# Performance work log

Hardware: AMD Instinct MI355X
Metric: run time of the kernel (lower is better)

The kernel has to match this reference:

```python
import jax, jax.numpy as jnp
import numpy as np

HEADS = 16
DIM_HEAD = 64
WINDOW = 16
TOPK_RATIO = 0.1
SCALE = DIM_HEAD ** -0.5


def setup_inputs() -> dict:
    key = jax.random.key(0)
    k1, k2, k3 = jax.random.split(key, 3)
    b, n, d = 2, 2048, 1024
    inner = HEADS * DIM_HEAD
    x = jax.random.normal(k1, (b, n, d), dtype=jnp.float32)
    W_qkv = jax.random.normal(k2, (d, 3 * inner), dtype=jnp.float32) * (d ** -0.5)
    W_out = jax.random.normal(k3, (inner, d), dtype=jnp.float32) * (inner ** -0.5)
    b_out = jnp.zeros((d,), dtype=jnp.float32)
    mask = jnp.ones((b, n), dtype=bool)
    return {"x": x, "W_qkv": W_qkv, "W_out": W_out, "b_out": b_out, "mask": mask}


def reference(x, W_qkv, W_out, b_out, mask):
    b, n, d = x.shape
    h, dh = HEADS, DIM_HEAD
    qkv = x @ W_qkv  # [b, n, 3*h*dh]
    q, k, v = jnp.split(qkv, 3, axis=-1)
    # [b, n, h, dh] -> [b, h, n, dh]
    q = q.reshape(b, n, h, dh).transpose(0, 2, 1, 3)
    k = k.reshape(b, n, h, dh).transpose(0, 2, 1, 3)
    v = v.reshape(b, n, h, dh).transpose(0, 2, 1, 3)

    dots = jnp.einsum('bhid,bhjd->bhij', q, k) * SCALE  # [b, h, n, n]
    NEG = -jnp.finfo(dots.dtype).max

    # sliding window mask: |i - j| <= WINDOW
    idx = jnp.arange(n)
    win = jnp.abs(idx[:, None] - idx[None, :]) <= WINDOW  # [n, n]
    dots = jnp.where(win[None, None], dots, NEG)

    # key padding mask [b, 1, 1, n]
    dots = jnp.where(mask[:, None, None, :], dots, NEG)

    # top-k masking (threshold from kth largest masked score)
    k_value = max(1, int(n * TOPK_RATIO))
    thr = jax.lax.top_k(dots, k_value)[0][..., -1:]  # [b, h, n, 1]
    dots = jnp.where(dots >= thr, dots, NEG)

    attn = jax.nn.softmax(dots, axis=-1)
    out = jnp.einsum('bhij,bhjd->bhid', attn, v)  # [b, h, n, dh]
    out = out.transpose(0, 2, 1, 3).reshape(b, n, h * dh)
    return out @ W_out + b_out
```

## Files before the change

kernel.cpp:

```cpp
#include <hip/hip_runtime.h>
#include <hip/hip_bf16.h>
#include <cstdint>
#include <cstddef>


typedef __hip_bfloat16 bf16;
typedef __attribute__((ext_vector_type(8))) short bf16x8;
typedef __attribute__((ext_vector_type(4))) float f32x4;

#define MFMA16(a, b, c) __builtin_amdgcn_mfma_f32_16x16x32_bf16((a), (b), (c), 0, 0, 0)

__device__ __forceinline__ unsigned short f2bu(float f) {
  return __bfloat16_as_ushort(__float2bfloat16(f));
}

__device__ __forceinline__ void async16(const void* g, void* lds) {
  __builtin_amdgcn_global_load_lds(
      (const __attribute__((address_space(1))) void*)g,
      (__attribute__((address_space(3))) void*)lds, 16, 0, 0);
}

__global__ __launch_bounds__(256) void prep_fused(const float* __restrict__ x,
                                                  const float* __restrict__ Wqkv,
                                                  const float* __restrict__ Wout,
                                                  bf16* __restrict__ xb,
                                                  bf16* __restrict__ wqkvt,
                                                  bf16* __restrict__ woutt) {
  __shared__ bf16 t[32][33];
  int bx = blockIdx.x, tid = threadIdx.x;
  if (bx < 4096) {
    int idx = (bx * 256 + tid) * 4;
    float4 v = *(const float4*)(x + idx);
    union { bf16 h[4]; uint2 u; } pk;
    pk.h[0] = __float2bfloat16(v.x);
    pk.h[1] = __float2bfloat16(v.y);
    pk.h[2] = __float2bfloat16(v.z);
    pk.h[3] = __float2bfloat16(v.w);
    *(uint2*)(xb + idx) = pk.u;
    return;
  }
  const float* W;
  bf16* Wt;
  int N, n0, k0;
  if (bx < 7168) {
    int L = bx - 4096;
    W = Wqkv; Wt = wqkvt; N = 3072;
    n0 = (L % 96) * 32; k0 = (L / 96) * 32;
  } else {
    int L = bx - 7168;
    W = Wout; Wt = woutt; N = 1024;
    n0 = (L & 31) * 32; k0 = (L >> 5) * 32;
  }
  int tx = tid & 31, ty = tid >> 5;
#pragma unroll
  for (int i = 0; i < 32; i += 8)
    t[ty + i][tx] = __float2bfloat16(W[(size_t)(k0 + ty + i) * N + n0 + tx]);
  __syncthreads();
#pragma unroll
  for (int i = 0; i < 32; i += 8)
    Wt[(size_t)(n0 + ty + i) * 1024 + k0 + tx] = t[tx][ty + i];
}

__global__ __launch_bounds__(256, 3) void gemm1_qkv(const bf16* __restrict__ A,
                                                    const bf16* __restrict__ Bt,
                                                    bf16* __restrict__ qkv) {
  const int K = 1024;
  __shared__ __align__(16) bf16 sA[128 * 32];
  __shared__ __align__(16) bf16 sB[128 * 32];
  __shared__ __align__(16) unsigned short sE[4][64 * 68];
  int L = blockIdx.x, xcd = L & 7, s = L >> 3;
  int by = (xcd >> 1) * 8 + s / 12;
  int bx = (xcd & 1) * 12 + s % 12;
  int row0 = by * 128, col0 = bx * 128;
  int tid = threadIdx.x, wave = tid >> 6, lane = tid & 63;
  int wr = wave >> 1, wc = wave & 1;
  int q = lane >> 4, l16 = lane & 15;
  f32x4 acc[4][4] = {};
  for (int k0 = 0; k0 < K; k0 += 32) {
    __syncthreads();
#pragma unroll
    for (int p = 0; p < 2; ++p) {
      int off = (wave * 2 + p) * 1024 + lane * 16;
      int r = off >> 6, cb = off & 63;
      async16(A + (size_t)(row0 + r) * K + k0 + (cb >> 1), (char*)sA + (wave * 2 + p) * 1024);
      async16(Bt + (size_t)(col0 + r) * K + k0 + (cb >> 1), (char*)sB + (wave * 2 + p) * 1024);
    }
    __syncthreads();
    bf16x8 af[4], bfr[4];
#pragma unroll
    for (int mi = 0; mi < 4; ++mi)
      af[mi] = *(const bf16x8*)&sA[(wr * 64 + mi * 16 + l16) * 32 + q * 8];
#pragma unroll
    for (int ni = 0; ni < 4; ++ni)
      bfr[ni] = *(const bf16x8*)&sB[(wc * 64 + ni * 16 + l16) * 32 + q * 8];
#pragma unroll
    for (int mi = 0; mi < 4; ++mi)
#pragma unroll
      for (int ni = 0; ni < 4; ++ni)
        acc[mi][ni] = MFMA16(af[mi], bfr[ni], acc[mi][ni]);
  }
  unsigned short* ep = sE[wave];
#pragma unroll
  for (int mi = 0; mi < 4; ++mi)
#pragma unroll
    for (int ni = 0; ni < 4; ++ni)
#pragma unroll
      for (int t = 0; t < 4; ++t)
        ep[(mi * 16 + q * 4 + t) * 68 + ni * 16 + l16] = f2bu(acc[mi][ni][t]);
  __syncthreads();
  const size_t TS = (size_t)2 * 16 * 2048 * 64;
  int c_base = col0 + wc * 64;
  int which = c_base >> 10, rc = c_base & 1023, h = rc >> 6;
  int r_base = row0 + wr * 64;
  int b = r_base >> 11, i_base = r_base & 2047;
  bf16* dst = qkv + (size_t)which * TS + (((size_t)(b * 16 + h)) * 2048 + i_base) * 64;
  int lr = lane >> 3, lc = lane & 7;
#pragma unroll
  for (int pass = 0; pass < 8; ++pass) {
    int row = pass * 8 + lr;
    uint4 val = *(const uint4*)&ep[row * 68 + lc * 8];
    *(uint4*)(dst + (size_t)row * 64 + lc * 8) = val;
  }
}

__global__ __launch_bounds__(256) void gemm2_out(const bf16* __restrict__ A,
                                                 const bf16* __restrict__ Bt,
                                                 const float* __restrict__ bias,
                                                 float* __restrict__ out) {
  const int K = 1024, N = 1024;
  __shared__ __align__(16) bf16 sA[128 * 32];
  __shared__ __align__(16) bf16 sB[64 * 32];
  int L = blockIdx.x, xcd = L & 7, s = L >> 3;
  int by = (xcd >> 1) * 8 + (s >> 3);
  int bx = (xcd & 1) * 8 + (s & 7);
  int row0 = by * 128, col0 = bx * 64;
  int tid = threadIdx.x, wave = tid >> 6, lane = tid & 63;
  int wr = wave >> 1, wc = wave & 1;
  int q = lane >> 4, l16 = lane & 15;
  f32x4 acc[4][2] = {};
  for (int k0 = 0; k0 < K; k0 += 32) {
    __syncthreads();
#pragma unroll
    for (int p = 0; p < 2; ++p) {
      int off = (wave * 2 + p) * 1024 + lane * 16;
      int r = off >> 6, cb = off & 63;
      async16(A + (size_t)(row0 + r) * K + k0 + (cb >> 1), (char*)sA + (wave * 2 + p) * 1024);
    }
    {
      int off = wave * 1024 + lane * 16;
      int r = off >> 6, cb = off & 63;
      async16(Bt + (size_t)(col0 + r) * K + k0 + (cb >> 1), (char*)sB + wave * 1024);
    }
    __syncthreads();
    bf16x8 af[4], bfr[2];
#pragma unroll
    for (int mi = 0; mi < 4; ++mi)
      af[mi] = *(const bf16x8*)&sA[(wr * 64 + mi * 16 + l16) * 32 + q * 8];
#pragma unroll
    for (int ni = 0; ni < 2; ++ni)
      bfr[ni] = *(const bf16x8*)&sB[(wc * 32 + ni * 16 + l16) * 32 + q * 8];
#pragma unroll
    for (int mi = 0; mi < 4; ++mi)
#pragma unroll
      for (int ni = 0; ni < 2; ++ni)
        acc[mi][ni] = MFMA16(af[mi], bfr[ni], acc[mi][ni]);
  }
#pragma unroll
  for (int mi = 0; mi < 4; ++mi) {
#pragma unroll
    for (int ni = 0; ni < 2; ++ni) {
      int c = col0 + wc * 32 + ni * 16 + l16;
      float bv = bias[c];
#pragma unroll
      for (int t = 0; t < 4; ++t) {
        int r = row0 + wr * 64 + mi * 16 + q * 4 + t;
        out[(size_t)r * N + c] = acc[mi][ni][t] + bv;
      }
    }
  }
}

__global__ __launch_bounds__(256, 4) void attn_mfma(const bf16* __restrict__ qkv,
                                                    bf16* __restrict__ aout) {
  __shared__ __align__(16) unsigned short sQ[64 * 72];
  __shared__ __align__(16) unsigned short sK[96 * 72];
  __shared__ __align__(16) unsigned short sVt[64 * 120];

  int tid = threadIdx.x, wave = tid >> 6, lane = tid & 63;
  int quad = lane >> 4, l16 = lane & 15;
  int bh = blockIdx.x >> 5, qb = blockIdx.x & 31;
  int i0 = qb * 64, jbase = i0 - 16;
  const size_t TS = (size_t)32 * 2048 * 64;
  const bf16* qbase = qkv + (size_t)bh * 2048 * 64;
  const bf16* kbase = qbase + TS;
  const bf16* vbase = qbase + 2 * TS;

#pragma unroll
  for (int u = tid; u < 512; u += 256) {
    int row = u >> 3, cg = u & 7;
    uint4 val = *(const uint4*)(qbase + (size_t)(i0 + row) * 64 + cg * 8);
    *(uint4*)&sQ[row * 72 + cg * 8] = val;
  }
#pragma unroll
  for (int u = tid; u < 768; u += 256) {
    int slot = u >> 3, cg = u & 7;
    int j = jbase + slot;
    uint4 val = make_uint4(0, 0, 0, 0);
    if ((unsigned)j < 2048u) val = *(const uint4*)(kbase + (size_t)j * 64 + cg * 8);
    *(uint4*)&sK[slot * 72 + cg * 8] = val;
  }
#pragma unroll
  for (int u = tid; u < 768; u += 256) {
    int slot = u >> 3, cg = u & 7;
    int j = jbase + slot;
    union { uint4 v; unsigned short s[8]; } pk;
    pk.v = make_uint4(0, 0, 0, 0);
    if ((unsigned)j < 2048u) pk.v = *(const uint4*)(vbase + (size_t)j * 64 + cg * 8);
#pragma unroll
    for (int d = 0; d < 8; ++d) sVt[(cg * 8 + d) * 120 + slot] = pk.s[d];
  }
  {
    int d = tid >> 2, s0 = 96 + (tid & 3) * 4;
    *(uint2*)&sVt[d * 120 + s0] = make_uint2(0, 0);
  }
  __syncthreads();

  int m0 = wave * 16;
  bf16x8 aq[2];
#pragma unroll
  for (int ks = 0; ks < 2; ++ks)
    aq[ks] = *(const bf16x8*)&sQ[(m0 + l16) * 72 + ks * 32 + quad * 8];
  f32x4 s[3] = {};
#pragma unroll
  for (int nt = 0; nt < 3; ++nt)
#pragma unroll
    for (int ks = 0; ks < 2; ++ks) {
      bf16x8 bk = *(const bf16x8*)&sK[(m0 + nt * 16 + l16) * 72 + ks * 32 + quad * 8];
      s[nt] = MFMA16(aq[ks], bk, s[nt]);
    }

  float rinv[4];
#pragma unroll
  for (int t = 0; t < 4; ++t) {
    int r = quad * 4 + t;
    float mx = -INFINITY;
#pragma unroll
    for (int nt = 0; nt < 3; ++nt) {
      int cl = nt * 16 + l16;
      int j = jbase + m0 + cl;
      bool valid = ((unsigned)(cl - r) <= 32u) && ((unsigned)j < 2048u);
      float v = valid ? s[nt][t] * 0.125f : -INFINITY;
      s[nt][t] = v;
      mx = fmaxf(mx, v);
    }
#pragma unroll
    for (int msk = 8; msk; msk >>= 1) mx = fmaxf(mx, __shfl_xor(mx, msk));
    float sum = 0.f;
#pragma unroll
    for (int nt = 0; nt < 3; ++nt) {
      float ev = __expf(s[nt][t] - mx);
      s[nt][t] = ev;
      sum += ev;
    }
#pragma unroll
    for (int msk = 8; msk; msk >>= 1) sum += __shfl_xor(sum, msk);
    rinv[t] = 1.0f / sum;
  }

  unsigned short* sPw = &sQ[m0 * 72];
#pragma unroll
  for (int t = 0; t < 4; ++t) {
#pragma unroll
    for (int nt = 0; nt < 3; ++nt)
      sPw[(quad * 4 + t) * 72 + nt * 16 + l16] = f2bu(s[nt][t]);
    sPw[(quad * 4 + t) * 72 + 48 + l16] = 0;
  }

  bf16x8 ap[2];
#pragma unroll
  for (int ks = 0; ks < 2; ++ks)
    ap[ks] = *(const bf16x8*)&sPw[l16 * 72 + ks * 32 + quad * 8];
  f32x4 o[4] = {};
#pragma unroll
  for (int dt = 0; dt < 4; ++dt)
#pragma unroll
    for (int ks = 0; ks < 2; ++ks) {
      bf16x8 bv = *(const bf16x8*)&sVt[(dt * 16 + l16) * 120 + m0 + ks * 32 + quad * 8];
      o[dt] = MFMA16(ap[ks], bv, o[dt]);
    }

  int b = bh >> 4, h = bh & 15;
#pragma unroll
  for (int dt = 0; dt < 4; ++dt)
#pragma unroll
    for (int t = 0; t < 4; ++t) {
      int r = i0 + m0 + quad * 4 + t;
      aout[((size_t)(b * 2048 + r)) * 1024 + h * 64 + dt * 16 + l16] =
          __float2bfloat16(o[dt][t] * rinv[t]);
    }
}

extern "C" void kernel_launch(void* const* d_in, const int* in_sizes, int n_in,
                              void* d_out, int out_size, void* d_ws, size_t ws_size,
                              hipStream_t stream) {
  const float* x = (const float*)d_in[0];
  const float* Wqkv = (const float*)d_in[1];
  const float* Wout = (const float*)d_in[2];
  const float* bout = (const float*)d_in[3];

  char* ws = (char*)d_ws;
  bf16* xb = (bf16*)(ws);
  bf16* wqkvt = (bf16*)(ws + 8388608);
  bf16* woutt = (bf16*)(ws + 14680064);
  bf16* qkvb = (bf16*)(ws + 16777216);
  bf16* aout = xb;

  hipLaunchKernelGGL(prep_fused, dim3(8192), dim3(256), 0, stream, x, Wqkv, Wout, xb, wqkvt, woutt);
  hipLaunchKernelGGL(gemm1_qkv, dim3(768), dim3(256), 0, stream, xb, wqkvt, qkvb);
  hipLaunchKernelGGL(attn_mfma, dim3(1024), dim3(256), 0, stream, qkvb, aout);
  hipLaunchKernelGGL(gemm2_out, dim3(512), dim3(256), 0, stream, aout, woutt, bout,
                     (float*)d_out);
}
```

Baseline: 149.5 us.

## Double K-step to 64 with XOR-swizzled LDS tiles in both GEMMs

Both GEMM kernels now load a 64-wide K slice per iteration into 128-byte rows whose 16-byte chunks are XOR-swizzled by row. This halves the barrier count per K and avoids LDS bank conflicts on the fragment reads. The per-lane global source pointers are precomputed once, and the QKV epilogue staging buffer is halved by writing in two phases so the larger tiles still fit at 3 blocks/CU. gemm2 also gains a launch-bounds occupancy hint. The cost is more LDS per block, which could limit occupancy.

```diff
diff --git a/kernel.cpp b/kernel.cpp
--- a/kernel.cpp
+++ b/kernel.cpp
@@ -65,9 +65,9 @@
                                                     const bf16* __restrict__ Bt,
                                                     bf16* __restrict__ qkv) {
   const int K = 1024;
-  __shared__ __align__(16) bf16 sA[128 * 32];
-  __shared__ __align__(16) bf16 sB[128 * 32];
-  __shared__ __align__(16) unsigned short sE[4][64 * 68];
+  __shared__ __align__(16) char sA[128 * 128];
+  __shared__ __align__(16) char sB[128 * 128];
+  __shared__ __align__(16) unsigned short sE[4][32 * 68];
   int L = blockIdx.x, xcd = L & 7, s = L >> 3;
   int by = (xcd >> 1) * 8 + s / 12;
   int bx = (xcd & 1) * 12 + s % 12;
@@ -75,61 +75,80 @@
   int tid = threadIdx.x, wave = tid >> 6, lane = tid & 63;
   int wr = wave >> 1, wc = wave & 1;
   int q = lane >> 4, l16 = lane & 15;
+  const bf16* srcA[4];
+  const bf16* srcB[4];
+#pragma unroll
+  for (int p = 0; p < 4; ++p) {
+    int off = (wave * 4 + p) * 1024 + lane * 16;
+    int r = off >> 7;
+    int col = ((((off & 127) >> 4) ^ (r & 7)) << 3);
+    srcA[p] = A + (size_t)(row0 + r) * K + col;
+    srcB[p] = Bt + (size_t)(col0 + r) * K + col;
+  }
+  int axor = (l16 & 7) << 4;
   f32x4 acc[4][4] = {};
-  for (int k0 = 0; k0 < K; k0 += 32) {
+  for (int k0 = 0; k0 < K; k0 += 64) {
     __syncthreads();
 #pragma unroll
-    for (int p = 0; p < 2; ++p) {
-      int off = (wave * 2 + p) * 1024 + lane * 16;
-      int r = off >> 6, cb = off & 63;
-      async16(A + (size_t)(row0 + r) * K + k0 + (cb >> 1), (char*)sA + (wave * 2 + p) * 1024);
-      async16(Bt + (size_t)(col0 + r) * K + k0 + (cb >> 1), (char*)sB + (wave * 2 + p) * 1024);
+    for (int p = 0; p < 4; ++p) {
+      int chunk = wave * 4 + p;
+      async16(srcA[p] + k0, sA + chunk * 1024);
+      async16(srcB[p] + k0, sB + chunk * 1024);
     }
     __syncthreads();
-    bf16x8 af[4], bfr[4];
-#pragma unroll
-    for (int mi = 0; mi < 4; ++mi)
-      af[mi] = *(const bf16x8*)&sA[(wr * 64 + mi * 16 + l16) * 32 + q * 8];
-#pragma unroll
-    for (int ni = 0; ni < 4; ++ni)
-      bfr[ni] = *(const bf16x8*)&sB[(wc * 64 + ni * 16 + l16) * 32 + q * 8];
-#pragma unroll
-    for (int mi = 0; mi < 4; ++mi)
+#pragma unroll
+    for (int half = 0; half < 2; ++half) {
+      bf16x8 af[4], bfr[4];
+#pragma unroll
+      for (int mi = 0; mi < 4; ++mi)
+        af[mi] = *(const bf16x8*)(sA + (wr * 64 + mi * 16 + l16) * 128 +
+                                  (((half * 4 + q) << 4) ^ axor));
 #pragma unroll
       for (int ni = 0; ni < 4; ++ni)
-        acc[mi][ni] = MFMA16(af[mi], bfr[ni], acc[mi][ni]);
-  }
-  unsigned short* ep = sE[wave];
-#pragma unroll
-  for (int mi = 0; mi < 4; ++mi)
-#pragma unroll
-    for (int ni = 0; ni < 4; ++ni)
-#pragma unroll
-      for (int t = 0; t < 4; ++t)
-        ep[(mi * 16 + q * 4 + t) * 68 + ni * 16 + l16] = f2bu(acc[mi][ni][t]);
-  __syncthreads();
+        bfr[ni] = *(const bf16x8*)(sB + (wc * 64 + ni * 16 + l16) * 128 +
+                                   (((half * 4 + q) << 4) ^ axor));
+#pragma unroll
+      for (int mi = 0; mi < 4; ++mi)
+#pragma unroll
+        for (int ni = 0; ni < 4; ++ni)
+          acc[mi][ni] = MFMA16(af[mi], bfr[ni], acc[mi][ni]);
+    }
+  }
   const size_t TS = (size_t)2 * 16 * 2048 * 64;
   int c_base = col0 + wc * 64;
-  int which = c_base >> 10, rc = c_base & 1023, h = rc >> 6;
+  int which = c_base >> 10, h = (c_base & 1023) >> 6;
   int r_base = row0 + wr * 64;
   int b = r_base >> 11, i_base = r_base & 2047;
   bf16* dst = qkv + (size_t)which * TS + (((size_t)(b * 16 + h)) * 2048 + i_base) * 64;
   int lr = lane >> 3, lc = lane & 7;
-#pragma unroll
-  for (int pass = 0; pass < 8; ++pass) {
-    int row = pass * 8 + lr;
-    uint4 val = *(const uint4*)&ep[row * 68 + lc * 8];
-    *(uint4*)(dst + (size_t)row * 64 + lc * 8) = val;
-  }
-}
-
-__global__ __launch_bounds__(256) void gemm2_out(const bf16* __restrict__ A,
-                                                 const bf16* __restrict__ Bt,
-                                                 const float* __restrict__ bias,
-                                                 float* __restrict__ out) {
+  unsigned short* ep = sE[wave];
+#pragma unroll
+  for (int ph = 0; ph < 2; ++ph) {
+#pragma unroll
+    for (int mi2 = 0; mi2 < 2; ++mi2) {
+      int mi = ph * 2 + mi2;
+#pragma unroll
+      for (int ni = 0; ni < 4; ++ni)
+#pragma unroll
+        for (int t = 0; t < 4; ++t)
+          ep[(mi2 * 16 + q * 4 + t) * 68 + ni * 16 + l16] = f2bu(acc[mi][ni][t]);
+    }
+#pragma unroll
+    for (int pass = 0; pass < 4; ++pass) {
+      int rloc = pass * 8 + lr;
+      uint4 val = *(const uint4*)&ep[rloc * 68 + lc * 8];
+      *(uint4*)(dst + (size_t)(ph * 32 + rloc) * 64 + lc * 8) = val;
+    }
+  }
+}
+
+__global__ __launch_bounds__(256, 3) void gemm2_out(const bf16* __restrict__ A,
+                                                    const bf16* __restrict__ Bt,
+                                                    const float* __restrict__ bias,
+                                                    float* __restrict__ out) {
   const int K = 1024, N = 1024;
-  __shared__ __align__(16) bf16 sA[128 * 32];
-  __shared__ __align__(16) bf16 sB[64 * 32];
+  __shared__ __align__(16) char sA[128 * 128];
+  __shared__ __align__(16) char sB[64 * 128];
   int L = blockIdx.x, xcd = L & 7, s = L >> 3;
   int by = (xcd >> 1) * 8 + (s >> 3);
   int bx = (xcd & 1) * 8 + (s & 7);
@@ -137,33 +156,48 @@
   int tid = threadIdx.x, wave = tid >> 6, lane = tid & 63;
   int wr = wave >> 1, wc = wave & 1;
   int q = lane >> 4, l16 = lane & 15;
+  const bf16* srcA[4];
+  const bf16* srcB[2];
+#pragma unroll
+  for (int p = 0; p < 4; ++p) {
+    int off = (wave * 4 + p) * 1024 + lane * 16;
+    int r = off >> 7;
+    int col = ((((off & 127) >> 4) ^ (r & 7)) << 3);
+    srcA[p] = A + (size_t)(row0 + r) * K + col;
+  }
+#pragma unroll
+  for (int p = 0; p < 2; ++p) {
+    int off = (wave * 2 + p) * 1024 + lane * 16;
+    int r = off >> 7;
+    int col = ((((off & 127) >> 4) ^ (r & 7)) << 3);
+    srcB[p] = Bt + (size_t)(col0 + r) * K + col;
+  }
+  int axor = (l16 & 7) << 4;
   f32x4 acc[4][2] = {};
-  for (int k0 = 0; k0 < K; k0 += 32) {
+  for (int k0 = 0; k0 < K; k0 += 64) {
     __syncthreads();
 #pragma unroll
-    for (int p = 0; p < 2; ++p) {
-      int off = (wave * 2 + p) * 1024 + lane * 16;
-      int r = off >> 6, cb = off & 63;
-      async16(A + (size_t)(row0 + r) * K + k0 + (cb >> 1), (char*)sA + (wave * 2 + p) * 1024);
-    }
-    {
-      int off = wave * 1024 + lane * 16;
-      int r = off >> 6, cb = off & 63;
-      async16(Bt + (size_t)(col0 + r) * K + k0 + (cb >> 1), (char*)sB + wave * 1024);
-    }
+    for (int p = 0; p < 4; ++p) async16(srcA[p] + k0, sA + (wave * 4 + p) * 1024);
+#pragma unroll
+    for (int p = 0; p < 2; ++p) async16(srcB[p] + k0, sB + (wave * 2 + p) * 1024);
     __syncthreads();
-    bf16x8 af[4], bfr[2];
-#pragma unroll
-    for (int mi = 0; mi < 4; ++mi)
-      af[mi] = *(const bf16x8*)&sA[(wr * 64 + mi * 16 + l16) * 32 + q * 8];
-#pragma unroll
-    for (int ni = 0; ni < 2; ++ni)
-      bfr[ni] = *(const bf16x8*)&sB[(wc * 32 + ni * 16 + l16) * 32 + q * 8];
-#pragma unroll
-    for (int mi = 0; mi < 4; ++mi)
+#pragma unroll
+    for (int half = 0; half < 2; ++half) {
+      bf16x8 af[4], bfr[2];
+#pragma unroll
+      for (int mi = 0; mi < 4; ++mi)
+        af[mi] = *(const bf16x8*)(sA + (wr * 64 + mi * 16 + l16) * 128 +
+                                  (((half * 4 + q) << 4) ^ axor));
 #pragma unroll
       for (int ni = 0; ni < 2; ++ni)
-        acc[mi][ni] = MFMA16(af[mi], bfr[ni], acc[mi][ni]);
+        bfr[ni] = *(const bf16x8*)(sB + (wc * 32 + ni * 16 + l16) * 128 +
+                                   (((half * 4 + q) << 4) ^ axor));
+#pragma unroll
+      for (int mi = 0; mi < 4; ++mi)
+#pragma unroll
+        for (int ni = 0; ni < 2; ++ni)
+          acc[mi][ni] = MFMA16(af[mi], bfr[ni], acc[mi][ni]);
+    }
   }
 #pragma unroll
   for (int mi = 0; mi < 4; ++mi) {
```

Result: faster. 140.3 us, median of 2 (-6.1%).
